# Kernel optimization log

Measured on AMD Instinct MI355X. Metric: run time of the kernel, lower is better.

## Reference

```python
import jax, jax.numpy as jnp
import numpy as np

H, D = 4, 64            # num_heads, head_size
HID = H * D             # 256
EPS = 1e-5              # torch LayerNorm default


def layer_norm(x, g, b):
    mu = x.mean(-1, keepdims=True)
    var = ((x - mu) ** 2).mean(-1, keepdims=True)
    return (x - mu) * jax.lax.rsqrt(var + EPS) * g + b


def mlstm_layer(x, Wq, Wk, Wv, Wo, bo, wi, bi, wf, bf, g, b):
    # x: (B, T, HID)
    B, T, _ = x.shape
    q = (x @ Wq).reshape(B, T, H, D) / (D ** 0.5)
    k = (x @ Wk).reshape(B, T, H, D)
    v = (x @ Wv).reshape(B, T, H, D)
    o = jax.nn.sigmoid(x @ Wo + bo).reshape(B, T, H, D)
    i_raw = x @ wi + bi  # (B, T, H)
    f_raw = x @ wf + bf  # (B, T, H)

    def step(carry, inp):
        C, n, m = carry                       # (B,H,D,D), (B,H,D), (B,H)
        q_t, k_t, v_t, o_t, i_t, f_t = inp
        m_t = jnp.maximum(f_t + m, i_t)       # stabilizer
        f_g = jnp.exp(f_t + m - m_t)          # (B,H)
        i_g = jnp.exp(i_t - m_t)              # (B,H)
        C = f_g[..., None, None] * C + i_g[..., None, None] * (v_t[..., :, None] * k_t[..., None, :])
        n = f_g[..., None] * n + i_g[..., None] * k_t
        Cq = jnp.einsum('bhde,bhd->bhe', C, q_t)
        nq = jnp.maximum(jnp.abs(jnp.sum(n * q_t, -1, keepdims=True)), 1.0)
        h = o_t * (Cq / nq)                   # (B,H,D)
        return (C, n, m_t), h.reshape(B, HID)

    C0 = jnp.zeros((B, H, D, D), x.dtype)
    n0 = jnp.zeros((B, H, D), x.dtype)
    m0 = jnp.zeros((B, H), x.dtype)
    xs = tuple(jnp.moveaxis(a, 1, 0) for a in (q, k, v, o, i_raw, f_raw))
    _, hs = jax.lax.scan(step, (C0, n0, m0), xs)  # hs: (T, B, HID)
    out = jnp.moveaxis(hs, 0, 1)                  # (B, T, HID)
    return layer_norm(out, g, b)


def setup_inputs() -> dict:
    B, T, IN, L = 256, 64, 170, 2
    key = jax.random.key(0)
    ks = jax.random.split(key, 19)
    s_in = 1.0 / np.sqrt(IN)
    s_h = 1.0 / np.sqrt(HID)
    return {
        'x':   jax.random.normal(ks[0], (B, T, IN), jnp.float32),
        'Wp':  jax.random.normal(ks[1], (IN, HID), jnp.float32) * s_in,
        'bp':  jax.random.normal(ks[2], (HID,), jnp.float32) * 0.01,
        'Wq':  jax.random.normal(ks[3], (L, HID, HID), jnp.float32) * s_h,
        'Wk':  jax.random.normal(ks[4], (L, HID, HID), jnp.float32) * s_h,
        'Wv':  jax.random.normal(ks[5], (L, HID, HID), jnp.float32) * s_h,
        'Wo':  jax.random.normal(ks[6], (L, HID, HID), jnp.float32) * s_h,
        'bo':  jax.random.normal(ks[7], (L, HID), jnp.float32) * 0.01,
        'wi':  jax.random.normal(ks[8], (L, HID, H), jnp.float32) * s_h,
        'bi':  jax.random.normal(ks[9], (L, H), jnp.float32) * 0.01,
        'wf':  jax.random.normal(ks[10], (L, HID, H), jnp.float32) * s_h,
        'bf':  jax.random.normal(ks[11], (L, H), jnp.float32) * 0.01,
        'lng': jnp.ones((L, HID), jnp.float32) + jax.random.normal(ks[12], (L, HID), jnp.float32) * 0.01,
        'lnb': jax.random.normal(ks[13], (L, HID), jnp.float32) * 0.01,
        'W1':  jax.random.normal(ks[14], (HID, 128), jnp.float32) * s_h,
        'b1':  jax.random.normal(ks[15], (128,), jnp.float32) * 0.01,
        'W2':  jax.random.normal(ks[16], (128, 2), jnp.float32) * (1.0 / np.sqrt(128)),
        'b2':  jax.random.normal(ks[17], (2,), jnp.float32) * 0.01,
    }


def reference(x, Wp, bp, Wq, Wk, Wv, Wo, bo, wi, bi, wf, bf, lng, lnb, W1, b1, W2, b2):
    h = x @ Wp + bp
    for l in range(Wq.shape[0]):
        h = mlstm_layer(h, Wq[l], Wk[l], Wv[l], Wo[l], bo[l],
                        wi[l], bi[l], wf[l], bf[l], lng[l], lnb[l])
    z = h[:, -1, :]                # last timestep
    z = jax.nn.relu(z @ W1 + b1)
    return z @ W2 + b2             # (B, 2)
```

## Files before the change

### kernel.cpp

```cpp
#include <hip/hip_runtime.h>
#include <math.h>

typedef __attribute__((ext_vector_type(4))) float f32x4;
typedef __attribute__((ext_vector_type(8))) short bf16x8;

constexpr int BATCH = 256;
constexpr int TT    = 64;
constexpr int NH    = 4;
constexpr int DH    = 64;
constexpr int HIDN  = 256;
constexpr int INDIM = 170;
constexpr int KPAD  = 192;
constexpr int ROWS  = BATCH * TT;
constexpr float EPS = 1e-5f;

#define MF(a, b, c) __builtin_amdgcn_mfma_f32_16x16x32_bf16((a), (b), (c), 0, 0, 0)

__device__ __forceinline__ unsigned short f2b(float f) {
    union { float f; unsigned int u; } v; v.f = f;
    return (unsigned short)((v.u + 0x7FFFu + ((v.u >> 16) & 1u)) >> 16);
}
__device__ __forceinline__ float b2f(unsigned short b) {
    union { unsigned int u; float f; } v; v.u = ((unsigned int)b) << 16;
    return v.f;
}
__device__ __forceinline__ void fsplit(float x, unsigned short& hi, unsigned short& lo) {
    hi = f2b(x);
    lo = f2b(x - b2f(hi));
}

__global__ __launch_bounds__(256) void pack_x(
    const float* __restrict__ x,
    unsigned short* __restrict__ xh, unsigned short* __restrict__ xl)
{
    int idx = blockIdx.x * 256 + threadIdx.x;
    if (idx >= ROWS * KPAD) return;
    int r = idx / KPAD, c = idx % KPAD;
    float v = (c < INDIM) ? x[(size_t)r * INDIM + c] : 0.f;
    unsigned short hi, lo; fsplit(v, hi, lo);
    xh[idx] = hi; xl[idx] = lo;
}

__global__ __launch_bounds__(256) void pack_w2(
    const float* __restrict__ Wp, const float* __restrict__ Wq,
    const float* __restrict__ Wk, const float* __restrict__ Wv,
    const float* __restrict__ Wo,
    unsigned short* __restrict__ WpTh, unsigned short* __restrict__ WpTl,
    unsigned short* __restrict__ Wth,  unsigned short* __restrict__ Wtl)
{
    __shared__ float T[64][65];
    const int t = blockIdx.x, tid = threadIdx.x;

    if (t < 128) {
        const int l = t >> 6, rem = t & 63;
        const int kt = rem >> 4, nt = rem & 15;
        const int n0 = nt * 64;
        const int seg = n0 >> 8, ns0 = n0 & 255;
        const float* W = (seg == 0) ? Wq : (seg == 1) ? Wk : (seg == 2) ? Wv : Wo;
        #pragma unroll
        for (int p = 0; p < 16; p++) {
            const int idx = p * 256 + tid;
            const int r = idx >> 6, c = idx & 63;
            T[r][c] = W[(size_t)l * 65536 + (size_t)(kt * 64 + r) * 256 + ns0 + c];
        }
        __syncthreads();
        #pragma unroll
        for (int p = 0; p < 16; p++) {
            const int idx = p * 256 + tid;
            const int nl = idx >> 6, kl = idx & 63;
            unsigned short hi, lo; fsplit(T[kl][nl], hi, lo);
            const size_t d = (size_t)l * 1024 * 256 + (size_t)(n0 + nl) * 256 + kt * 64 + kl;
            Wth[d] = hi; Wtl[d] = lo;
        }
    } else {
        const int t2 = t - 128;
        const int kt = t2 % 3, nt = t2 / 3;
        #pragma unroll
        for (int p = 0; p < 16; p++) {
            const int idx = p * 256 + tid;
            const int r = idx >> 6, c = idx & 63;
            const int k = kt * 64 + r;
            T[r][c] = (k < INDIM) ? Wp[(size_t)k * HIDN + nt * 64 + c] : 0.f;
        }
        __syncthreads();
        #pragma unroll
        for (int p = 0; p < 16; p++) {
            const int idx = p * 256 + tid;
            const int nl = idx >> 6, kl = idx & 63;
            unsigned short hi, lo; fsplit(T[kl][nl], hi, lo);
            const size_t d = (size_t)(nt * 64 + nl) * KPAD + kt * 64 + kl;
            WpTh[d] = hi; WpTl[d] = lo;
        }
    }
}

__global__ __launch_bounds__(256) void gemm_mfma3(
    const unsigned short* __restrict__ Ah, const unsigned short* __restrict__ Al,
    const unsigned short* __restrict__ Bh, const unsigned short* __restrict__ Bl,
    const float* __restrict__ bias,
    unsigned short* __restrict__ c0, unsigned short* __restrict__ c1,
    int M, int N, int K)
{
    __shared__ unsigned short AsH[128 * 64];
    __shared__ unsigned short AsL[128 * 64];
    __shared__ unsigned short BsH[128 * 64];
    __shared__ unsigned short BsL[128 * 64];
    const int tid  = threadIdx.x;
    const int lane = tid & 63;
    const int wave = tid >> 6;
    const int wr = wave >> 1, wc = wave & 1;
    const int m0 = blockIdx.x * 128, n0 = blockIdx.y * 128;

    f32x4 acc[4][4] = {};

    for (int k0 = 0; k0 < K; k0 += 64) {
        #pragma unroll
        for (int j = 0; j < 4; j++) {
            int c   = j * 256 + tid;
            int row = c >> 3;
            int kcs = ((c & 7) ^ (row & 7)) * 8;
            size_t aoff = (size_t)(m0 + row) * K + k0 + kcs;
            size_t boff = (size_t)(n0 + row) * K + k0 + kcs;
            __builtin_amdgcn_global_load_lds(
                (const __attribute__((address_space(1))) void*)(Ah + aoff),
                (__attribute__((address_space(3))) void*)(AsH + c * 8), 16, 0, 0);
            __builtin_amdgcn_global_load_lds(
                (const __attribute__((address_space(1))) void*)(Al + aoff),
                (__attribute__((address_space(3))) void*)(AsL + c * 8), 16, 0, 0);
            __builtin_amdgcn_global_load_lds(
                (const __attribute__((address_space(1))) void*)(Bh + boff),
                (__attribute__((address_space(3))) void*)(BsH + c * 8), 16, 0, 0);
            __builtin_amdgcn_global_load_lds(
                (const __attribute__((address_space(1))) void*)(Bl + boff),
                (__attribute__((address_space(3))) void*)(BsL + c * 8), 16, 0, 0);
        }
        asm volatile("s_waitcnt vmcnt(0)" ::: "memory");
        __syncthreads();

        #pragma unroll
        for (int kk = 0; kk < 2; kk++) {
            bf16x8 ah[4], al[4], bh[4], bl[4];
            #pragma unroll
            for (int i = 0; i < 4; i++) {
                const int ar  = wr * 64 + i * 16 + (lane & 15);
                const int off = ar * 64 + (((kk * 4 + (lane >> 4)) ^ (ar & 7)) * 8);
                ah[i] = *(const bf16x8*)&AsH[off];
                al[i] = *(const bf16x8*)&AsL[off];
            }
            #pragma unroll
            for (int j = 0; j < 4; j++) {
                const int br  = wc * 64 + j * 16 + (lane & 15);
                const int off = br * 64 + (((kk * 4 + (lane >> 4)) ^ (br & 7)) * 8);
                bh[j] = *(const bf16x8*)&BsH[off];
                bl[j] = *(const bf16x8*)&BsL[off];
            }
            #pragma unroll
            for (int i = 0; i < 4; i++) {
                #pragma unroll
                for (int j = 0; j < 4; j++) {
                    acc[i][j] = MF(ah[i], bh[j], acc[i][j]);
                    acc[i][j] = MF(ah[i], bl[j], acc[i][j]);
                    acc[i][j] = MF(al[i], bh[j], acc[i][j]);
                }
            }
        }
        __syncthreads();
    }

    #pragma unroll
    for (int i = 0; i < 4; i++) {
        #pragma unroll
        for (int j = 0; j < 4; j++) {
            const int col = n0 + wc * 64 + j * 16 + (lane & 15);
            const float bv = bias[col];
            #pragma unroll
            for (int r = 0; r < 4; r++) {
                const int row = m0 + wr * 64 + i * 16 + (lane >> 4) * 4 + r;
                float v = acc[i][j][r] + bv;
                unsigned short hi, lo; fsplit(v, hi, lo);
                c0[(size_t)row * N + col] = hi;
                c1[(size_t)row * N + col] = lo;
            }
        }
    }
}

__global__ __launch_bounds__(256) void ifproj(
    const unsigned short* __restrict__ hbh, const unsigned short* __restrict__ hbl,
    const float* __restrict__ wi, const float* __restrict__ wf,
    const float* __restrict__ bi, const float* __restrict__ bf,
    float* __restrict__ iout, float* __restrict__ fout)
{
    const int w    = threadIdx.x >> 6;
    const int lane = threadIdx.x & 63;
    const int row  = blockIdx.x * 4 + w;
    ushort4 a4 = *(const ushort4*)(hbh + (size_t)row * HIDN + lane * 4);
    ushort4 l4 = *(const ushort4*)(hbl + (size_t)row * HIDN + lane * 4);
    float yv[4];
    yv[0] = b2f(a4.x) + b2f(l4.x);
    yv[1] = b2f(a4.y) + b2f(l4.y);
    yv[2] = b2f(a4.z) + b2f(l4.z);
    yv[3] = b2f(a4.w) + b2f(l4.w);

    float g8[8] = {0.f,0.f,0.f,0.f,0.f,0.f,0.f,0.f};
    #pragma unroll
    for (int j = 0; j < 4; j++) {
        const float4 wiv = *(const float4*)(wi + (size_t)(lane * 4 + j) * 4);
        const float4 wfv = *(const float4*)(wf + (size_t)(lane * 4 + j) * 4);
        g8[0] += yv[j] * wiv.x; g8[1] += yv[j] * wiv.y;
        g8[2] += yv[j] * wiv.z; g8[3] += yv[j] * wiv.w;
        g8[4] += yv[j] * wfv.x; g8[5] += yv[j] * wfv.y;
        g8[6] += yv[j] * wfv.z; g8[7] += yv[j] * wfv.w;
    }
    #pragma unroll
    for (int o = 0; o < 8; o++)
        #pragma unroll
        for (int off = 32; off; off >>= 1) g8[o] += __shfl_xor(g8[o], off);
    if (lane < 4)      iout[(size_t)row * NH + lane] = g8[lane] + bi[lane];
    else if (lane < 8) fout[(size_t)row * NH + lane - 4] = g8[lane] + bf[lane - 4];
}

__global__ __launch_bounds__(512, 4) void fused_layer(
    const unsigned short* __restrict__ Ah, const unsigned short* __restrict__ Al,
    const unsigned short* __restrict__ Bh, const unsigned short* __restrict__ Bl,
    const float* __restrict__ bo,
    const float* __restrict__ irg, const float* __restrict__ frg,
    unsigned short* __restrict__ hoh, unsigned short* __restrict__ hol)
{
    extern __shared__ char smem[];
    unsigned short* const S = (unsigned short*)smem;
    float* const Ot   = (float*)smem;
    float* const denF = (float*)(S + 18432);

    const int n0  = blockIdx.x;
    const int mm  = n0 >> 3;
    const int hh  = mm & 3;
    const int b   = (n0 & 7) + 8 * (mm >> 2);
    const int tid = threadIdx.x, lane = tid & 63, w = tid >> 6;

    float iv = irg[(size_t)(b * TT + lane) * NH + hh];
    float fv = frg[(size_t)(b * TT + lane) * NH + hh];
    float F = fv;
    #pragma unroll
    for (int d2 = 1; d2 < 64; d2 <<= 1) { float o2 = __shfl_up(F, d2); if (lane >= d2) F += o2; }
    const float sa_r = iv - F;
    float pm = sa_r;
    #pragma unroll
    for (int d2 = 1; d2 < 64; d2 <<= 1) { float o2 = __shfl_up(pm, d2); if (lane >= d2) pm = fmaxf(pm, o2); }
    const float sc_r = -fmaxf(0.f, pm);

    const int wm = w >> 2, wn = w & 3;

    const unsigned short* sptr0; const unsigned short* sptr1;
    const unsigned short* sptr2; const unsigned short* sptr3;
    const unsigned short* sptr4;
    int sdst0, sdst1, sdst2, sdst3, sdst4;
    {
        {
            const int hl = tid >> 8, c = tid & 255;
            const int r = c >> 2, cp = c & 3;
            const int col = (cp ^ ((r >> 1) & 3)) * 8;
            sptr0 = (hl ? Al : Ah) + (size_t)(b * TT + r) * 256 + col;
            sdst0 = hl * 2048 + c * 8;
        }
        #pragma unroll
        for (int rr = 0; rr < 4; rr++) {
            const int c2 = rr * 512 + tid;
            const int hl = c2 >> 10, c = c2 & 1023;
            const int r = c >> 2, cp = c & 3;
            const int grow = (r >> 6) * 256 + hh * 64 + (r & 63);
            const int col = (cp ^ ((r >> 1) & 3)) * 8;
            const unsigned short* p = (hl ? Bl : Bh) + (size_t)grow * 256 + col;
            const int d = 4096 + hl * 8192 + c * 8;
            if (rr == 0) { sptr1 = p; sdst1 = d; }
            else if (rr == 1) { sptr2 = p; sdst2 = d; }
            else if (rr == 2) { sptr3 = p; sdst3 = d; }
            else { sptr4 = p; sdst4 = d; }
        }
    }

#define STAGE(bs)                                                              \
    do {                                                                       \
        __builtin_amdgcn_global_load_lds(                                      \
            (const __attribute__((address_space(1))) void*)sptr0,              \
            (__attribute__((address_space(3))) void*)(S + (bs) + sdst0), 16, 0, 0); \
        __builtin_amdgcn_global_load_lds(                                      \
            (const __attribute__((address_space(1))) void*)sptr1,              \
            (__attribute__((address_space(3))) void*)(S + (bs) + sdst1), 16, 0, 0); \
        __builtin_amdgcn_global_load_lds(                                      \
            (const __attribute__((address_space(1))) void*)sptr2,              \
            (__attribute__((address_space(3))) void*)(S + (bs) + sdst2), 16, 0, 0); \
        __builtin_amdgcn_global_load_lds(                                      \
            (const __attribute__((address_space(1))) void*)sptr3,              \
            (__attribute__((address_space(3))) void*)(S + (bs) + sdst3), 16, 0, 0); \
        __builtin_amdgcn_global_load_lds(                                      \
            (const __attribute__((address_space(1))) void*)sptr4,              \
            (__attribute__((address_space(3))) void*)(S + (bs) + sdst4), 16, 0, 0); \
        sptr0 += 32; sptr1 += 32; sptr2 += 32; sptr3 += 32; sptr4 += 32;       \
    } while (0)

    int aoff_[2], boff_[4];
    #pragma unroll
    for (int i = 0; i < 2; i++) {
        const int ar = wm * 32 + i * 16 + (lane & 15);
        aoff_[i] = ar * 32 + (((lane >> 4) ^ ((ar >> 1) & 3)) * 8);
    }
    #pragma unroll
    for (int j = 0; j < 4; j++) {
        const int br = wn * 64 + j * 16 + (lane & 15);
        boff_[j] = br * 32 + (((lane >> 4) ^ ((br >> 1) & 3)) * 8);
    }

    STAGE(0);
    asm volatile("s_waitcnt vmcnt(0)" ::: "memory");
    __syncthreads();

    f32x4 acc[2][4] = {};
    #pragma unroll
    for (int s = 0; s < 8; s++) {
        if (s < 7) STAGE(((s + 1) & 1) * 20480);

        const int pb = (s & 1) * 20480;
        __builtin_amdgcn_s_setprio(1);
        bf16x8 a_h[2], a_l[2], b_h[4], b_l[4];
        #pragma unroll
        for (int i = 0; i < 2; i++) {
            a_h[i] = *(const bf16x8*)&S[pb + aoff_[i]];
            a_l[i] = *(const bf16x8*)&S[pb + 2048 + aoff_[i]];
        }
        #pragma unroll
        for (int j = 0; j < 4; j++) {
            b_h[j] = *(const bf16x8*)&S[pb + 4096 + boff_[j]];
            b_l[j] = *(const bf16x8*)&S[pb + 12288 + boff_[j]];
        }
        #pragma unroll
        for (int i = 0; i < 2; i++) {
            #pragma unroll
            for (int j = 0; j < 4; j++) {
                acc[i][j] = MF(a_h[i], b_h[j], acc[i][j]);
                acc[i][j] = MF(a_h[i], b_l[j], acc[i][j]);
                acc[i][j] = MF(a_l[i], b_h[j], acc[i][j]);
            }
        }
        __builtin_amdgcn_s_setprio(0);
        if (s < 7) {
            asm volatile("s_waitcnt vmcnt(0)" ::: "memory");
            __syncthreads();
        }
    }
    __syncthreads();
#undef STAGE

    const int colb = lane & 15;
    const int rowb = (lane >> 4) * 4;
    #pragma unroll
    for (int i = 0; i < 2; i++) {
        #pragma unroll
        for (int j = 0; j < 4; j++) {
            const int d = j * 16 + colb;
            #pragma unroll
            for (int r = 0; r < 4; r++) {
                const int t = wm * 32 + i * 16 + rowb + r;
                float v = acc[i][j][r];
                if (wn == 0) {
                    v *= 0.125f;
                    unsigned short hi, lo; fsplit(v, hi, lo);
                    const int idx = t * 64 + (d ^ ((t & 7) << 3));
                    S[8192 + idx] = hi; S[12288 + idx] = lo;
                } else if (wn == 1) {
                    unsigned short hi, lo; fsplit(v, hi, lo);
                    const int idx = t * 64 + (d ^ ((t & 7) << 3));
                    S[16384 + idx] = hi; S[20480 + idx] = lo;
                    const int idx2 = d * 64 + (t ^ ((d & 7) << 3));
                    S[24576 + idx2] = hi; S[28672 + idx2] = lo;
                } else if (wn == 2) {
                    unsigned short hi, lo; fsplit(v, hi, lo);
                    const int idx = t * 64 + (d ^ ((t & 7) << 3));
                    S[32768 + idx] = hi; S[36864 + idx] = lo;
                } else {
                    Ot[t * 64 + d] = 1.f / (1.f + __expf(-(v + bo[hh * 64 + d])));
                }
            }
        }
    }
    __syncthreads();

    const int tg = w & 3, sh = w >> 2;
    f32x4 sv[2] = {}, sk[2] = {};
    const int tA = tg * 16 + (lane & 15);
    #pragma unroll
    for (int kk = 0; kk < 2; kk++) {
        const int eA = (kk * 32 + (lane >> 4) * 8) ^ ((tA & 7) << 3);
        bf16x8 aQh = *(const bf16x8*)&S[8192  + tA * 64 + eA];
        bf16x8 aQl = *(const bf16x8*)&S[12288 + tA * 64 + eA];
        #pragma unroll
        for (int j = 0; j < 2; j++) {
            const int sB = sh * 32 + j * 16 + (lane & 15);
            const int eB = (kk * 32 + (lane >> 4) * 8) ^ ((sB & 7) << 3);
            bf16x8 bKh = *(const bf16x8*)&S[16384 + sB * 64 + eB];
            bf16x8 bKl = *(const bf16x8*)&S[20480 + sB * 64 + eB];
            bf16x8 bVh = *(const bf16x8*)&S[32768 + sB * 64 + eB];
            bf16x8 bVl = *(const bf16x8*)&S[36864 + sB * 64 + eB];
            sv[j] = MF(aQh, bVh, sv[j]);
            sv[j] = MF(aQh, bVl, sv[j]);
            sv[j] = MF(aQl, bVh, sv[j]);
            sk[j] = MF(aQh, bKh, sk[j]);
            sk[j] = MF(aQh, bKl, sk[j]);
            sk[j] = MF(aQl, bKh, sk[j]);
        }
    }

    const int tbase = tg * 16 + (lane >> 4) * 4;
    float cw[4], dh4[4] = {0.f, 0.f, 0.f, 0.f};
    #pragma unroll
    for (int r = 0; r < 4; r++) cw[r] = __shfl(sc_r, tbase + r);
    #pragma unroll
    for (int j = 0; j < 2; j++) {
        const int s = sh * 32 + j * 16 + (lane & 15);
        const float as = __shfl(sa_r, s);
        #pragma unroll
        for (int r = 0; r < 4; r++) {
            const int t = tbase + r;
            const float wgt = (s <= t) ? __expf(as + cw[r]) : 0.f;
            sv[j][r] *= wgt;
            dh4[r] += sk[j][r] * wgt;
        }
    }
    #pragma unroll
    for (int r = 0; r < 4; r++) {
        dh4[r] += __shfl_xor(dh4[r], 1);
        dh4[r] += __shfl_xor(dh4[r], 2);
        dh4[r] += __shfl_xor(dh4[r], 4);
        dh4[r] += __shfl_xor(dh4[r], 8);
    }

    __syncthreads();

    #pragma unroll
    for (int j = 0; j < 2; j++) {
        const int s = sh * 32 + j * 16 + (lane & 15);
        #pragma unroll
        for (int r = 0; r < 4; r++) {
            const int t = tbase + r;
            unsigned short hi, lo; fsplit(sv[j][r], hi, lo);
            S[8192  + t * 72 + s] = hi;
            S[12800 + t * 72 + s] = lo;
        }
    }
    if ((lane & 15) == 0) {
        #pragma unroll
        for (int r = 0; r < 4; r++) denF[sh * 64 + tbase + r] = dh4[r];
    }
    __syncthreads();

    f32x4 num[2] = {};
    #pragma unroll
    for (int kk = 0; kk < 2; kk++) {
        const int sA2 = kk * 32 + (lane >> 4) * 8;
        bf16x8 aPh = *(const bf16x8*)&S[8192  + tA * 72 + sA2];
        bf16x8 aPl = *(const bf16x8*)&S[12800 + tA * 72 + sA2];
        #pragma unroll
        for (int j = 0; j < 2; j++) {
            const int e2 = sh * 32 + j * 16 + (lane & 15);
            const int tB = (kk * 32 + (lane >> 4) * 8) ^ ((e2 & 7) << 3);
            bf16x8 bTh = *(const bf16x8*)&S[24576 + e2 * 64 + tB];
            bf16x8 bTl = *(const bf16x8*)&S[28672 + e2 * 64 + tB];
            num[j] = MF(aPh, bTh, num[j]);
            num[j] = MF(aPh, bTl, num[j]);
            num[j] = MF(aPl, bTh, num[j]);
        }
    }

    #pragma unroll
    for (int j = 0; j < 2; j++) {
        const int e = sh * 32 + j * 16 + (lane & 15);
        #pragma unroll
        for (int r = 0; r < 4; r++) {
            const int t = tbase + r;
            const float den = fmaxf(fabsf(denF[t] + denF[64 + t]), 1.f);
            const float o = Ot[t * 64 + e];
            const float hval = o * num[j][r] / den;
            unsigned short hi, lo; fsplit(hval, hi, lo);
            const size_t oidx = (size_t)(b * TT + t) * HIDN + hh * DH + e;
            hoh[oidx] = hi; hol[oidx] = lo;
        }
    }
}

__global__ __launch_bounds__(256) void layernorm_gate(
    const unsigned short* __restrict__ sh_, const unsigned short* __restrict__ sl_,
    unsigned short* __restrict__ dh_, unsigned short* __restrict__ dl_,
    const float* __restrict__ g, const float* __restrict__ bta,
    const float* __restrict__ wi, const float* __restrict__ wf,
    const float* __restrict__ bi, const float* __restrict__ bf,
    float* __restrict__ iout, float* __restrict__ fout)
{
    const int w    = threadIdx.x >> 6;
    const int lane = threadIdx.x & 63;
    const int row  = blockIdx.x * 4 + w;
    ushort4 a4 = *(const ushort4*)(sh_ + (size_t)row * HIDN + lane * 4);
    ushort4 l4 = *(const ushort4*)(sl_ + (size_t)row * HIDN + lane * 4);
    float x0 = b2f(a4.x) + b2f(l4.x);
    float x1 = b2f(a4.y) + b2f(l4.y);
    float x2 = b2f(a4.z) + b2f(l4.z);
    float x3 = b2f(a4.w) + b2f(l4.w);
    float s = x0 + x1 + x2 + x3;
    #pragma unroll
    for (int off = 32; off; off >>= 1) s += __shfl_xor(s, off);
    const float mu = s * (1.f / 256.f);
    const float d0 = x0 - mu, d1 = x1 - mu, d2 = x2 - mu, d3 = x3 - mu;
    float vs = d0*d0 + d1*d1 + d2*d2 + d3*d3;
    #pragma unroll
    for (int off = 32; off; off >>= 1) vs += __shfl_xor(vs, off);
    const float rstd = rsqrtf(vs * (1.f / 256.f) + EPS);
    const float4 gv = *(const float4*)(g + lane * 4);
    const float4 bv = *(const float4*)(bta + lane * 4);
    float yv[4];
    yv[0] = d0 * rstd * gv.x + bv.x;
    yv[1] = d1 * rstd * gv.y + bv.y;
    yv[2] = d2 * rstd * gv.z + bv.z;
    yv[3] = d3 * rstd * gv.w + bv.w;
    ushort4 h4, o4;
    fsplit(yv[0], h4.x, o4.x); fsplit(yv[1], h4.y, o4.y);
    fsplit(yv[2], h4.z, o4.z); fsplit(yv[3], h4.w, o4.w);
    *(ushort4*)(dh_ + (size_t)row * HIDN + lane * 4) = h4;
    *(ushort4*)(dl_ + (size_t)row * HIDN + lane * 4) = o4;

    if (wi) {
        float g8[8] = {0.f,0.f,0.f,0.f,0.f,0.f,0.f,0.f};
        #pragma unroll
        for (int j = 0; j < 4; j++) {
            const float4 wiv = *(const float4*)(wi + (size_t)(lane * 4 + j) * 4);
            const float4 wfv = *(const float4*)(wf + (size_t)(lane * 4 + j) * 4);
            g8[0] += yv[j] * wiv.x; g8[1] += yv[j] * wiv.y;
            g8[2] += yv[j] * wiv.z; g8[3] += yv[j] * wiv.w;
            g8[4] += yv[j] * wfv.x; g8[5] += yv[j] * wfv.y;
            g8[6] += yv[j] * wfv.z; g8[7] += yv[j] * wfv.w;
        }
        #pragma unroll
        for (int o = 0; o < 8; o++)
            #pragma unroll
            for (int off = 32; off; off >>= 1) g8[o] += __shfl_xor(g8[o], off);
        if (lane < 4)      iout[(size_t)row * NH + lane] = g8[lane] + bi[lane];
        else if (lane < 8) fout[(size_t)row * NH + lane - 4] = g8[lane] + bf[lane - 4];
    }
}

__global__ __launch_bounds__(128) void head_mlp(
    const unsigned short* __restrict__ hbh, const unsigned short* __restrict__ hbl,
    const float* __restrict__ W1, const float* __restrict__ b1,
    const float* __restrict__ W2, const float* __restrict__ b2,
    float* __restrict__ out)
{
    const int b = blockIdx.x;
    const int j = threadIdx.x;
    __shared__ float z[HIDN];
    __shared__ float a[128];
    const size_t rb = ((size_t)b * TT + (TT - 1)) * HIDN;
    z[j]       = b2f(hbh[rb + j])       + b2f(hbl[rb + j]);
    z[j + 128] = b2f(hbh[rb + j + 128]) + b2f(hbl[rb + j + 128]);
    __syncthreads();
    float acc = b1[j];
    #pragma unroll 4
    for (int c = 0; c < HIDN; c++) acc += z[c] * W1[c * 128 + j];
    a[j] = fmaxf(acc, 0.f);
    __syncthreads();
    if (j < 2) {
        float s = b2[j];
        for (int c = 0; c < 128; c++) s += a[c] * W2[c * 2 + j];
        out[b * 2 + j] = s;
    }
}

extern "C" void kernel_launch(void* const* d_in, const int* in_sizes, int n_in,
                              void* d_out, int out_size, void* d_ws, size_t ws_size,
                              hipStream_t stream)
{
    const float* x   = (const float*)d_in[0];
    const float* Wp  = (const float*)d_in[1];
    const float* bp  = (const float*)d_in[2];
    const float* Wq  = (const float*)d_in[3];
    const float* Wk  = (const float*)d_in[4];
    const float* Wv  = (const float*)d_in[5];
    const float* Wo  = (const float*)d_in[6];
    const float* bo  = (const float*)d_in[7];
    const float* wi  = (const float*)d_in[8];
    const float* bi  = (const float*)d_in[9];
    const float* wf  = (const float*)d_in[10];
    const float* bf  = (const float*)d_in[11];
    const float* lng = (const float*)d_in[12];
    const float* lnb = (const float*)d_in[13];
    const float* W1  = (const float*)d_in[14];
    const float* b1  = (const float*)d_in[15];
    const float* W2  = (const float*)d_in[16];
    const float* b2  = (const float*)d_in[17];
    float* out = (float*)d_out;

    unsigned short* hbh = (unsigned short*)d_ws;
    unsigned short* hbl = hbh + (size_t)ROWS * HIDN;
    unsigned short* h2h = hbl + (size_t)ROWS * HIDN;
    unsigned short* h2l = h2h + (size_t)ROWS * HIDN;
    float*          ir  = (float*)(h2l + (size_t)ROWS * HIDN);
    float*          fr  = ir + (size_t)ROWS * NH;
    unsigned short* WpTh = (unsigned short*)(fr + (size_t)ROWS * NH);
    unsigned short* WpTl = WpTh + (size_t)HIDN * KPAD;
    unsigned short* Wth  = WpTl + (size_t)HIDN * KPAD;
    unsigned short* Wtl  = Wth + (size_t)2 * 1024 * 256;
    unsigned short* xh = h2h;
    unsigned short* xl = h2l;

    pack_x<<<(ROWS * KPAD + 255) / 256, 256, 0, stream>>>(x, xh, xl);
    pack_w2<<<140, 256, 0, stream>>>(Wp, Wq, Wk, Wv, Wo, WpTh, WpTl, Wth, Wtl);

    gemm_mfma3<<<dim3(128, 2), 256, 0, stream>>>(
        xh, xl, WpTh, WpTl, bp, hbh, hbl, ROWS, HIDN, KPAD);

    ifproj<<<ROWS / 4, 256, 0, stream>>>(hbh, hbl, wi, wf, bi, bf, ir, fr);

    fused_layer<<<BATCH * NH, 512, 81920, stream>>>(
        hbh, hbl, Wth, Wtl, bo, ir, fr, h2h, h2l);
    layernorm_gate<<<ROWS / 4, 256, 0, stream>>>(
        h2h, h2l, hbh, hbl, lng, lnb,
        wi + (size_t)HIDN * NH, wf + (size_t)HIDN * NH, bi + NH, bf + NH, ir, fr);

    fused_layer<<<BATCH * NH, 512, 81920, stream>>>(
        hbh, hbl, Wth + (size_t)1024 * 256, Wtl + (size_t)1024 * 256,
        bo + HIDN, ir, fr, h2h, h2l);
    layernorm_gate<<<ROWS / 4, 256, 0, stream>>>(
        h2h, h2l, hbh, hbl, lng + HIDN, lnb + HIDN,
        nullptr, nullptr, nullptr, nullptr, nullptr, nullptr);

    head_mlp<<<BATCH, 128, 0, stream>>>(hbh, hbl, W1, b1, W2, b2, out);
}
```

Measured before the change: 169.9 us.

## Process four batches per block in fused_layer to reuse weight tiles

Each fused_layer block now handles four batch elements for one head instead of one. The projection GEMM stages a single weight tile per K step and reuses it across four A tiles, so weight traffic into LDS per batch drops. The grid shrinks from 1024 to 256 blocks, LDS per block grows to 128KB, and the accumulators grow to 4x2x4 MFMA tiles. The per-batch chunkwise mLSTM epilogue runs serially inside the block, which costs parallelism and occupancy.

```diff
diff --git a/kernel.cpp b/kernel.cpp
--- a/kernel.cpp
+++ b/kernel.cpp
@@ -220,7 +220,7 @@
     else if (lane < 8) fout[(size_t)row * NH + lane - 4] = g8[lane] + bf[lane - 4];
 }
 
-__global__ __launch_bounds__(512, 4) void fused_layer(
+__global__ __launch_bounds__(512, 2) void fused_layer(
     const unsigned short* __restrict__ Ah, const unsigned short* __restrict__ Al,
     const unsigned short* __restrict__ Bh, const unsigned short* __restrict__ Bl,
     const float* __restrict__ bo,
@@ -232,114 +232,106 @@
     float* const Ot   = (float*)smem;
     float* const denF = (float*)(S + 18432);
 
-    const int n0  = blockIdx.x;
-    const int mm  = n0 >> 3;
-    const int hh  = mm & 3;
-    const int b   = (n0 & 7) + 8 * (mm >> 2);
+    const int bid = blockIdx.x;
+    const int hh  = (bid >> 3) & 3;
+    const int bg  = (bid & 7) + 8 * (bid >> 5);
+    const int b0  = bg * 4;
     const int tid = threadIdx.x, lane = tid & 63, w = tid >> 6;
 
-    float iv = irg[(size_t)(b * TT + lane) * NH + hh];
-    float fv = frg[(size_t)(b * TT + lane) * NH + hh];
-    float F = fv;
-    #pragma unroll
-    for (int d2 = 1; d2 < 64; d2 <<= 1) { float o2 = __shfl_up(F, d2); if (lane >= d2) F += o2; }
-    const float sa_r = iv - F;
-    float pm = sa_r;
-    #pragma unroll
-    for (int d2 = 1; d2 < 64; d2 <<= 1) { float o2 = __shfl_up(pm, d2); if (lane >= d2) pm = fmaxf(pm, o2); }
-    const float sc_r = -fmaxf(0.f, pm);
+    float sa4[4], sc4[4];
+    #pragma unroll
+    for (int g = 0; g < 4; g++) {
+        float iv = irg[(size_t)((b0 + g) * TT + lane) * NH + hh];
+        float fv = frg[(size_t)((b0 + g) * TT + lane) * NH + hh];
+        float F = fv;
+        #pragma unroll
+        for (int d2 = 1; d2 < 64; d2 <<= 1) { float o2 = __shfl_up(F, d2); if (lane >= d2) F += o2; }
+        const float av = iv - F;
+        float pm = av;
+        #pragma unroll
+        for (int d2 = 1; d2 < 64; d2 <<= 1) { float o2 = __shfl_up(pm, d2); if (lane >= d2) pm = fmaxf(pm, o2); }
+        sa4[g] = av;
+        sc4[g] = -fmaxf(0.f, pm);
+    }
 
     const int wm = w >> 2, wn = w & 3;
 
-    const unsigned short* sptr0; const unsigned short* sptr1;
-    const unsigned short* sptr2; const unsigned short* sptr3;
-    const unsigned short* sptr4;
-    int sdst0, sdst1, sdst2, sdst3, sdst4;
-    {
-        {
-            const int hl = tid >> 8, c = tid & 255;
-            const int r = c >> 2, cp = c & 3;
-            const int col = (cp ^ ((r >> 1) & 3)) * 8;
-            sptr0 = (hl ? Al : Ah) + (size_t)(b * TT + r) * 256 + col;
-            sdst0 = hl * 2048 + c * 8;
-        }
-        #pragma unroll
-        for (int rr = 0; rr < 4; rr++) {
-            const int c2 = rr * 512 + tid;
-            const int hl = c2 >> 10, c = c2 & 1023;
-            const int r = c >> 2, cp = c & 3;
-            const int grow = (r >> 6) * 256 + hh * 64 + (r & 63);
-            const int col = (cp ^ ((r >> 1) & 3)) * 8;
-            const unsigned short* p = (hl ? Bl : Bh) + (size_t)grow * 256 + col;
-            const int d = 4096 + hl * 8192 + c * 8;
-            if (rr == 0) { sptr1 = p; sdst1 = d; }
-            else if (rr == 1) { sptr2 = p; sdst2 = d; }
-            else if (rr == 2) { sptr3 = p; sdst3 = d; }
-            else { sptr4 = p; sdst4 = d; }
-        }
+    const unsigned short* sp[8];
+    unsigned int sd[8];
+    #pragma unroll
+    for (int q = 0; q < 8; q++) {
+        const int c  = q * 512 + tid;
+        const int rg = c >> 10;
+        const int cc = c & 1023;
+        const int r  = cc >> 2;
+        const int cp = cc & 3;
+        const int colsw = (cp ^ ((r >> 1) & 3)) * 8;
+        size_t grow;
+        const unsigned short* base;
+        if (rg < 2) { base = (rg == 0) ? Ah : Al; grow = (size_t)(bg * 256 + r); }
+        else {
+            base = (rg == 2) ? Bh : Bl;
+            grow = (size_t)((r >> 6) * 256 + hh * 64 + (r & 63));
+        }
+        sp[q] = base + grow * 256 + colsw;
+        sd[q] = rg * 8192 + cc * 8;
     }
 
 #define STAGE(bs)                                                              \
     do {                                                                       \
-        __builtin_amdgcn_global_load_lds(                                      \
-            (const __attribute__((address_space(1))) void*)sptr0,              \
-            (__attribute__((address_space(3))) void*)(S + (bs) + sdst0), 16, 0, 0); \
-        __builtin_amdgcn_global_load_lds(                                      \
-            (const __attribute__((address_space(1))) void*)sptr1,              \
-            (__attribute__((address_space(3))) void*)(S + (bs) + sdst1), 16, 0, 0); \
-        __builtin_amdgcn_global_load_lds(                                      \
-            (const __attribute__((address_space(1))) void*)sptr2,              \
-            (__attribute__((address_space(3))) void*)(S + (bs) + sdst2), 16, 0, 0); \
-        __builtin_amdgcn_global_load_lds(                                      \
-            (const __attribute__((address_space(1))) void*)sptr3,              \
-            (__attribute__((address_space(3))) void*)(S + (bs) + sdst3), 16, 0, 0); \
-        __builtin_amdgcn_global_load_lds(                                      \
-            (const __attribute__((address_space(1))) void*)sptr4,              \
-            (__attribute__((address_space(3))) void*)(S + (bs) + sdst4), 16, 0, 0); \
-        sptr0 += 32; sptr1 += 32; sptr2 += 32; sptr3 += 32; sptr4 += 32;       \
+        _Pragma("unroll")                                                      \
+        for (int q = 0; q < 8; q++) {                                          \
+            __builtin_amdgcn_global_load_lds(                                  \
+                (const __attribute__((address_space(1))) void*)sp[q],          \
+                (__attribute__((address_space(3))) void*)(S + (bs) + sd[q]), 16, 0, 0); \
+            sp[q] += 32;                                                       \
+        }                                                                      \
     } while (0)
 
-    int aoff_[2], boff_[4];
+    unsigned int aoffb[2], boffb[4];
     #pragma unroll
     for (int i = 0; i < 2; i++) {
         const int ar = wm * 32 + i * 16 + (lane & 15);
-        aoff_[i] = ar * 32 + (((lane >> 4) ^ ((ar >> 1) & 3)) * 8);
+        aoffb[i] = ar * 32 + (((lane >> 4) ^ ((ar >> 1) & 3)) * 8);
     }
     #pragma unroll
     for (int j = 0; j < 4; j++) {
         const int br = wn * 64 + j * 16 + (lane & 15);
-        boff_[j] = br * 32 + (((lane >> 4) ^ ((br >> 1) & 3)) * 8);
+        boffb[j] = br * 32 + (((lane >> 4) ^ ((br >> 1) & 3)) * 8);
     }
 
     STAGE(0);
     asm volatile("s_waitcnt vmcnt(0)" ::: "memory");
     __syncthreads();
 
-    f32x4 acc[2][4] = {};
-    #pragma unroll
+    f32x4 acc[4][2][4] = {};
     for (int s = 0; s < 8; s++) {
-        if (s < 7) STAGE(((s + 1) & 1) * 20480);
-
-        const int pb = (s & 1) * 20480;
+        if (s < 7) STAGE(((s + 1) & 1) * 32768);
+
+        const int pb = (s & 1) * 32768;
         __builtin_amdgcn_s_setprio(1);
-        bf16x8 a_h[2], a_l[2], b_h[4], b_l[4];
-        #pragma unroll
-        for (int i = 0; i < 2; i++) {
-            a_h[i] = *(const bf16x8*)&S[pb + aoff_[i]];
-            a_l[i] = *(const bf16x8*)&S[pb + 2048 + aoff_[i]];
-        }
+        bf16x8 b_h[4], b_l[4];
         #pragma unroll
         for (int j = 0; j < 4; j++) {
-            b_h[j] = *(const bf16x8*)&S[pb + 4096 + boff_[j]];
-            b_l[j] = *(const bf16x8*)&S[pb + 12288 + boff_[j]];
-        }
-        #pragma unroll
-        for (int i = 0; i < 2; i++) {
-            #pragma unroll
-            for (int j = 0; j < 4; j++) {
-                acc[i][j] = MF(a_h[i], b_h[j], acc[i][j]);
-                acc[i][j] = MF(a_h[i], b_l[j], acc[i][j]);
-                acc[i][j] = MF(a_l[i], b_h[j], acc[i][j]);
+            b_h[j] = *(const bf16x8*)&S[pb + 16384 + boffb[j]];
+            b_l[j] = *(const bf16x8*)&S[pb + 24576 + boffb[j]];
+        }
+        #pragma unroll
+        for (int g = 0; g < 4; g++) {
+            bf16x8 a_h[2], a_l[2];
+            #pragma unroll
+            for (int i = 0; i < 2; i++) {
+                a_h[i] = *(const bf16x8*)&S[pb + g * 2048 + aoffb[i]];
+                a_l[i] = *(const bf16x8*)&S[pb + 8192 + g * 2048 + aoffb[i]];
+            }
+            #pragma unroll
+            for (int i = 0; i < 2; i++) {
+                #pragma unroll
+                for (int j = 0; j < 4; j++) {
+                    acc[g][i][j] = MF(a_h[i], b_h[j], acc[g][i][j]);
+                    acc[g][i][j] = MF(a_h[i], b_l[j], acc[g][i][j]);
+                    acc[g][i][j] = MF(a_l[i], b_h[j], acc[g][i][j]);
+                }
             }
         }
         __builtin_amdgcn_s_setprio(0);
@@ -353,137 +345,144 @@
 
     const int colb = lane & 15;
     const int rowb = (lane >> 4) * 4;
-    #pragma unroll
-    for (int i = 0; i < 2; i++) {
-        #pragma unroll
-        for (int j = 0; j < 4; j++) {
-            const int d = j * 16 + colb;
+    const int tg = w & 3, sh = w >> 2;
+    const int tA = tg * 16 + (lane & 15);
+    const int tbase = tg * 16 + (lane >> 4) * 4;
+
+    #pragma unroll
+    for (int g = 0; g < 4; g++) {
+        const int bcur = b0 + g;
+
+        #pragma unroll
+        for (int i = 0; i < 2; i++) {
+            #pragma unroll
+            for (int j = 0; j < 4; j++) {
+                const int d = j * 16 + colb;
+                #pragma unroll
+                for (int r = 0; r < 4; r++) {
+                    const int t = wm * 32 + i * 16 + rowb + r;
+                    float v = acc[g][i][j][r];
+                    if (wn == 0) {
+                        v *= 0.125f;
+                        unsigned short hi, lo; fsplit(v, hi, lo);
+                        const int idx = t * 64 + (d ^ ((t & 7) << 3));
+                        S[8192 + idx] = hi; S[12288 + idx] = lo;
+                    } else if (wn == 1) {
+                        unsigned short hi, lo; fsplit(v, hi, lo);
+                        const int idx = t * 64 + (d ^ ((t & 7) << 3));
+                        S[16384 + idx] = hi; S[20480 + idx] = lo;
+                        const int idx2 = d * 64 + (t ^ ((d & 7) << 3));
+                        S[24576 + idx2] = hi; S[28672 + idx2] = lo;
+                    } else if (wn == 2) {
+                        unsigned short hi, lo; fsplit(v, hi, lo);
+                        const int idx = t * 64 + (d ^ ((t & 7) << 3));
+                        S[32768 + idx] = hi; S[36864 + idx] = lo;
+                    } else {
+                        Ot[t * 64 + d] = 1.f / (1.f + __expf(-(v + bo[hh * 64 + d])));
+                    }
+                }
+            }
+        }
+        __syncthreads();
+
+        f32x4 sv[2] = {}, sk[2] = {};
+        #pragma unroll
+        for (int kk = 0; kk < 2; kk++) {
+            const int eA = (kk * 32 + (lane >> 4) * 8) ^ ((tA & 7) << 3);
+            bf16x8 aQh = *(const bf16x8*)&S[8192  + tA * 64 + eA];
+            bf16x8 aQl = *(const bf16x8*)&S[12288 + tA * 64 + eA];
+            #pragma unroll
+            for (int j = 0; j < 2; j++) {
+                const int sB = sh * 32 + j * 16 + (lane & 15);
+                const int eB = (kk * 32 + (lane >> 4) * 8) ^ ((sB & 7) << 3);
+                bf16x8 bKh = *(const bf16x8*)&S[16384 + sB * 64 + eB];
+                bf16x8 bKl = *(const bf16x8*)&S[20480 + sB * 64 + eB];
+                bf16x8 bVh = *(const bf16x8*)&S[32768 + sB * 64 + eB];
+                bf16x8 bVl = *(const bf16x8*)&S[36864 + sB * 64 + eB];
+                sv[j] = MF(aQh, bVh, sv[j]);
+                sv[j] = MF(aQh, bVl, sv[j]);
+                sv[j] = MF(aQl, bVh, sv[j]);
+                sk[j] = MF(aQh, bKh, sk[j]);
+                sk[j] = MF(aQh, bKl, sk[j]);
+                sk[j] = MF(aQl, bKh, sk[j]);
+            }
+        }
+
+        float cw[4], dh4[4] = {0.f, 0.f, 0.f, 0.f};
+        #pragma unroll
+        for (int r = 0; r < 4; r++) cw[r] = __shfl(sc4[g], tbase + r);
+        #pragma unroll
+        for (int j = 0; j < 2; j++) {
+            const int s = sh * 32 + j * 16 + (lane & 15);
+            const float as = __shfl(sa4[g], s);
             #pragma unroll
             for (int r = 0; r < 4; r++) {
-                const int t = wm * 32 + i * 16 + rowb + r;
-                float v = acc[i][j][r];
-                if (wn == 0) {
-                    v *= 0.125f;
-                    unsigned short hi, lo; fsplit(v, hi, lo);
-                    const int idx = t * 64 + (d ^ ((t & 7) << 3));
-                    S[8192 + idx] = hi; S[12288 + idx] = lo;
-                } else if (wn == 1) {
-                    unsigned short hi, lo; fsplit(v, hi, lo);
-                    const int idx = t * 64 + (d ^ ((t & 7) << 3));
-                    S[16384 + idx] = hi; S[20480 + idx] = lo;
-                    const int idx2 = d * 64 + (t ^ ((d & 7) << 3));
-                    S[24576 + idx2] = hi; S[28672 + idx2] = lo;
-                } else if (wn == 2) {
-                    unsigned short hi, lo; fsplit(v, hi, lo);
-                    const int idx = t * 64 + (d ^ ((t & 7) << 3));
-                    S[32768 + idx] = hi; S[36864 + idx] = lo;
-                } else {
-                    Ot[t * 64 + d] = 1.f / (1.f + __expf(-(v + bo[hh * 64 + d])));
-                }
-            }
-        }
-    }
-    __syncthreads();
-
-    const int tg = w & 3, sh = w >> 2;
-    f32x4 sv[2] = {}, sk[2] = {};
-    const int tA = tg * 16 + (lane & 15);
-    #pragma unroll
-    for (int kk = 0; kk < 2; kk++) {
-        const int eA = (kk * 32 + (lane >> 4) * 8) ^ ((tA & 7) << 3);
-        bf16x8 aQh = *(const bf16x8*)&S[8192  + tA * 64 + eA];
-        bf16x8 aQl = *(const bf16x8*)&S[12288 + tA * 64 + eA];
+                const int t = tbase + r;
+                const float wgt = (s <= t) ? __expf(as + cw[r]) : 0.f;
+                sv[j][r] *= wgt;
+                dh4[r] += sk[j][r] * wgt;
+            }
+        }
+        #pragma unroll
+        for (int r = 0; r < 4; r++) {
+            dh4[r] += __shfl_xor(dh4[r], 1);
+            dh4[r] += __shfl_xor(dh4[r], 2);
+            dh4[r] += __shfl_xor(dh4[r], 4);
+            dh4[r] += __shfl_xor(dh4[r], 8);
+        }
+
+        __syncthreads();
+
         #pragma unroll
         for (int j = 0; j < 2; j++) {
-            const int sB = sh * 32 + j * 16 + (lane & 15);
-            const int eB = (kk * 32 + (lane >> 4) * 8) ^ ((sB & 7) << 3);
-            bf16x8 bKh = *(const bf16x8*)&S[16384 + sB * 64 + eB];
-            bf16x8 bKl = *(const bf16x8*)&S[20480 + sB * 64 + eB];
-            bf16x8 bVh = *(const bf16x8*)&S[32768 + sB * 64 + eB];
-            bf16x8 bVl = *(const bf16x8*)&S[36864 + sB * 64 + eB];
-            sv[j] = MF(aQh, bVh, sv[j]);
-            sv[j] = MF(aQh, bVl, sv[j]);
-            sv[j] = MF(aQl, bVh, sv[j]);
-            sk[j] = MF(aQh, bKh, sk[j]);
-            sk[j] = MF(aQh, bKl, sk[j]);
-            sk[j] = MF(aQl, bKh, sk[j]);
-        }
-    }
-
-    const int tbase = tg * 16 + (lane >> 4) * 4;
-    float cw[4], dh4[4] = {0.f, 0.f, 0.f, 0.f};
-    #pragma unroll
-    for (int r = 0; r < 4; r++) cw[r] = __shfl(sc_r, tbase + r);
-    #pragma unroll
-    for (int j = 0; j < 2; j++) {
-        const int s = sh * 32 + j * 16 + (lane & 15);
-        const float as = __shfl(sa_r, s);
-        #pragma unroll
-        for (int r = 0; r < 4; r++) {
-            const int t = tbase + r;
-            const float wgt = (s <= t) ? __expf(as + cw[r]) : 0.f;
-            sv[j][r] *= wgt;
-            dh4[r] += sk[j][r] * wgt;
-        }
-    }
-    #pragma unroll
-    for (int r = 0; r < 4; r++) {
-        dh4[r] += __shfl_xor(dh4[r], 1);
-        dh4[r] += __shfl_xor(dh4[r], 2);
-        dh4[r] += __shfl_xor(dh4[r], 4);
-        dh4[r] += __shfl_xor(dh4[r], 8);
-    }
-
-    __syncthreads();
-
-    #pragma unroll
-    for (int j = 0; j < 2; j++) {
-        const int s = sh * 32 + j * 16 + (lane & 15);
-        #pragma unroll
-        for (int r = 0; r < 4; r++) {
-            const int t = tbase + r;
-            unsigned short hi, lo; fsplit(sv[j][r], hi, lo);
-            S[8192  + t * 72 + s] = hi;
-            S[12800 + t * 72 + s] = lo;
-        }
-    }
-    if ((lane & 15) == 0) {
-        #pragma unroll
-        for (int r = 0; r < 4; r++) denF[sh * 64 + tbase + r] = dh4[r];
-    }
-    __syncthreads();
-
-    f32x4 num[2] = {};
-    #pragma unroll
-    for (int kk = 0; kk < 2; kk++) {
-        const int sA2 = kk * 32 + (lane >> 4) * 8;
-        bf16x8 aPh = *(const bf16x8*)&S[8192  + tA * 72 + sA2];
-        bf16x8 aPl = *(const bf16x8*)&S[12800 + tA * 72 + sA2];
+            const int s = sh * 32 + j * 16 + (lane & 15);
+            #pragma unroll
+            for (int r = 0; r < 4; r++) {
+                const int t = tbase + r;
+                unsigned short hi, lo; fsplit(sv[j][r], hi, lo);
+                S[8192  + t * 72 + s] = hi;
+                S[12800 + t * 72 + s] = lo;
+            }
+        }
+        if ((lane & 15) == 0) {
+            #pragma unroll
+            for (int r = 0; r < 4; r++) denF[sh * 64 + tbase + r] = dh4[r];
+        }
+        __syncthreads();
+
+        f32x4 num[2] = {};
+        #pragma unroll
+        for (int kk = 0; kk < 2; kk++) {
+            const int sA2 = kk * 32 + (lane >> 4) * 8;
+            bf16x8 aPh = *(const bf16x8*)&S[8192  + tA * 72 + sA2];
+            bf16x8 aPl = *(const bf16x8*)&S[12800 + tA * 72 + sA2];
+            #pragma unroll
+            for (int j = 0; j < 2; j++) {
+                const int e2 = sh * 32 + j * 16 + (lane & 15);
+                const int tB = (kk * 32 + (lane >> 4) * 8) ^ ((e2 & 7) << 3);
+                bf16x8 bTh = *(const bf16x8*)&S[24576 + e2 * 64 + tB];
+                bf16x8 bTl = *(const bf16x8*)&S[28672 + e2 * 64 + tB];
+                num[j] = MF(aPh, bTh, num[j]);
+                num[j] = MF(aPh, bTl, num[j]);
+                num[j] = MF(aPl, bTh, num[j]);
+            }
+        }
+
         #pragma unroll
         for (int j = 0; j < 2; j++) {
-            const int e2 = sh * 32 + j * 16 + (lane & 15);
-            const int tB = (kk * 32 + (lane >> 4) * 8) ^ ((e2 & 7) << 3);
-            bf16x8 bTh = *(const bf16x8*)&S[24576 + e2 * 64 + tB];
-            bf16x8 bTl = *(const bf16x8*)&S[28672 + e2 * 64 + tB];
-            num[j] = MF(aPh, bTh, num[j]);
-            num[j] = MF(aPh, bTl, num[j]);
-            num[j] = MF(aPl, bTh, num[j]);
-        }
-    }
-
-    #pragma unroll
-    for (int j = 0; j < 2; j++) {
-        const int e = sh * 32 + j * 16 + (lane & 15);
-        #pragma unroll
-        for (int r = 0; r < 4; r++) {
-            const int t = tbase + r;
-            const float den = fmaxf(fabsf(denF[t] + denF[64 + t]), 1.f);
-            const float o = Ot[t * 64 + e];
-            const float hval = o * num[j][r] / den;
-            unsigned short hi, lo; fsplit(hval, hi, lo);
-            const size_t oidx = (size_t)(b * TT + t) * HIDN + hh * DH + e;
-            hoh[oidx] = hi; hol[oidx] = lo;
-        }
+            const int e = sh * 32 + j * 16 + (lane & 15);
+            #pragma unroll
+            for (int r = 0; r < 4; r++) {
+                const int t = tbase + r;
+                const float den = fmaxf(fabsf(denF[t] + denF[64 + t]), 1.f);
+                const float o = Ot[t * 64 + e];
+                const float hval = o * num[j][r] / den;
+                unsigned short hi, lo; fsplit(hval, hi, lo);
+                const size_t oidx = (size_t)(bcur * TT + t) * HIDN + hh * DH + e;
+                hoh[oidx] = hi; hol[oidx] = lo;
+            }
+        }
+        __syncthreads();
     }
 }
 
@@ -617,13 +616,13 @@
 
     ifproj<<<ROWS / 4, 256, 0, stream>>>(hbh, hbl, wi, wf, bi, bf, ir, fr);
 
-    fused_layer<<<BATCH * NH, 512, 81920, stream>>>(
+    fused_layer<<<256, 512, 131072, stream>>>(
         hbh, hbl, Wth, Wtl, bo, ir, fr, h2h, h2l);
     layernorm_gate<<<ROWS / 4, 256, 0, stream>>>(
         h2h, h2l, hbh, hbl, lng, lnb,
         wi + (size_t)HIDN * NH, wf + (size_t)HIDN * NH, bi + NH, bf + NH, ir, fr);
 
-    fused_layer<<<BATCH * NH, 512, 81920, stream>>>(
+    fused_layer<<<256, 512, 131072, stream>>>(
         hbh, hbl, Wth + (size_t)1024 * 256, Wtl + (size_t)1024 * 256,
         bo + HIDN, ir, fr, h2h, h2l);
     layernorm_gate<<<ROWS / 4, 256, 0, stream>>>(
```

After: 529.8 us. 212% more time.

## Use single-bf16 intra-chunk attention and single-buffer staging to raise occupancy

Applied to the files above, without the earlier changes.

Replaces the hi/lo split-bf16 (three-MFMA) products for QK, QV and P·K^T inside the fused layer with single bf16 operands and one MFMA each. It also drops the double-buffered global-to-LDS staging of the projection GEMM in favour of a single buffer with sync per step. Together these shrink dynamic LDS from 80 KB to 48 KB, and launch bounds are raised to allow more blocks per CU. The aim is fewer MFMAs, less LDS traffic and higher occupancy. The cost is lower numerical precision in the recurrence math and lost load/compute overlap in the GEMM loop.

```diff
diff --git a/kernel.cpp b/kernel.cpp
--- a/kernel.cpp
+++ b/kernel.cpp
@@ -220,7 +220,7 @@
     else if (lane < 8) fout[(size_t)row * NH + lane - 4] = g8[lane] + bf[lane - 4];
 }
 
-__global__ __launch_bounds__(512, 4) void fused_layer(
+__global__ __launch_bounds__(512, 6) void fused_layer(
     const unsigned short* __restrict__ Ah, const unsigned short* __restrict__ Al,
     const unsigned short* __restrict__ Bh, const unsigned short* __restrict__ Bl,
     const float* __restrict__ bo,
@@ -230,7 +230,7 @@
     extern __shared__ char smem[];
     unsigned short* const S = (unsigned short*)smem;
     float* const Ot   = (float*)smem;
-    float* const denF = (float*)(S + 18432);
+    float* const denF = (float*)(S + 12800);
 
     const int n0  = blockIdx.x;
     const int mm  = n0 >> 3;
@@ -279,23 +279,23 @@
         }
     }
 
-#define STAGE(bs)                                                              \
+#define STAGE()                                                                \
     do {                                                                       \
         __builtin_amdgcn_global_load_lds(                                      \
             (const __attribute__((address_space(1))) void*)sptr0,              \
-            (__attribute__((address_space(3))) void*)(S + (bs) + sdst0), 16, 0, 0); \
+            (__attribute__((address_space(3))) void*)(S + sdst0), 16, 0, 0);   \
         __builtin_amdgcn_global_load_lds(                                      \
             (const __attribute__((address_space(1))) void*)sptr1,              \
-            (__attribute__((address_space(3))) void*)(S + (bs) + sdst1), 16, 0, 0); \
+            (__attribute__((address_space(3))) void*)(S + sdst1), 16, 0, 0);   \
         __builtin_amdgcn_global_load_lds(                                      \
             (const __attribute__((address_space(1))) void*)sptr2,              \
-            (__attribute__((address_space(3))) void*)(S + (bs) + sdst2), 16, 0, 0); \
+            (__attribute__((address_space(3))) void*)(S + sdst2), 16, 0, 0);   \
         __builtin_amdgcn_global_load_lds(                                      \
             (const __attribute__((address_space(1))) void*)sptr3,              \
-            (__attribute__((address_space(3))) void*)(S + (bs) + sdst3), 16, 0, 0); \
+            (__attribute__((address_space(3))) void*)(S + sdst3), 16, 0, 0);   \
         __builtin_amdgcn_global_load_lds(                                      \
             (const __attribute__((address_space(1))) void*)sptr4,              \
-            (__attribute__((address_space(3))) void*)(S + (bs) + sdst4), 16, 0, 0); \
+            (__attribute__((address_space(3))) void*)(S + sdst4), 16, 0, 0);   \
         sptr0 += 32; sptr1 += 32; sptr2 += 32; sptr3 += 32; sptr4 += 32;       \
     } while (0)
 
@@ -311,27 +311,23 @@
         boff_[j] = br * 32 + (((lane >> 4) ^ ((br >> 1) & 3)) * 8);
     }
 
-    STAGE(0);
-    asm volatile("s_waitcnt vmcnt(0)" ::: "memory");
-    __syncthreads();
-
     f32x4 acc[2][4] = {};
-    #pragma unroll
     for (int s = 0; s < 8; s++) {
-        if (s < 7) STAGE(((s + 1) & 1) * 20480);
-
-        const int pb = (s & 1) * 20480;
+        STAGE();
+        asm volatile("s_waitcnt vmcnt(0)" ::: "memory");
+        __syncthreads();
+
         __builtin_amdgcn_s_setprio(1);
         bf16x8 a_h[2], a_l[2], b_h[4], b_l[4];
         #pragma unroll
         for (int i = 0; i < 2; i++) {
-            a_h[i] = *(const bf16x8*)&S[pb + aoff_[i]];
-            a_l[i] = *(const bf16x8*)&S[pb + 2048 + aoff_[i]];
+            a_h[i] = *(const bf16x8*)&S[aoff_[i]];
+            a_l[i] = *(const bf16x8*)&S[2048 + aoff_[i]];
         }
         #pragma unroll
         for (int j = 0; j < 4; j++) {
-            b_h[j] = *(const bf16x8*)&S[pb + 4096 + boff_[j]];
-            b_l[j] = *(const bf16x8*)&S[pb + 12288 + boff_[j]];
+            b_h[j] = *(const bf16x8*)&S[4096 + boff_[j]];
+            b_l[j] = *(const bf16x8*)&S[12288 + boff_[j]];
         }
         #pragma unroll
         for (int i = 0; i < 2; i++) {
@@ -343,12 +339,8 @@
             }
         }
         __builtin_amdgcn_s_setprio(0);
-        if (s < 7) {
-            asm volatile("s_waitcnt vmcnt(0)" ::: "memory");
-            __syncthreads();
-        }
-    }
-    __syncthreads();
+        __syncthreads();
+    }
 #undef STAGE
 
     const int colb = lane & 15;
@@ -363,20 +355,17 @@
                 const int t = wm * 32 + i * 16 + rowb + r;
                 float v = acc[i][j][r];
                 if (wn == 0) {
-                    v *= 0.125f;
-                    unsigned short hi, lo; fsplit(v, hi, lo);
                     const int idx = t * 64 + (d ^ ((t & 7) << 3));
-                    S[8192 + idx] = hi; S[12288 + idx] = lo;
+                    S[8192 + idx] = f2b(v * 0.125f);
                 } else if (wn == 1) {
-                    unsigned short hi, lo; fsplit(v, hi, lo);
+                    const unsigned short kb = f2b(v);
                     const int idx = t * 64 + (d ^ ((t & 7) << 3));
-                    S[16384 + idx] = hi; S[20480 + idx] = lo;
+                    S[12288 + idx] = kb;
                     const int idx2 = d * 64 + (t ^ ((d & 7) << 3));
-                    S[24576 + idx2] = hi; S[28672 + idx2] = lo;
+                    S[16384 + idx2] = kb;
                 } else if (wn == 2) {
-                    unsigned short hi, lo; fsplit(v, hi, lo);
                     const int idx = t * 64 + (d ^ ((t & 7) << 3));
-                    S[32768 + idx] = hi; S[36864 + idx] = lo;
+                    S[20480 + idx] = f2b(v);
                 } else {
                     Ot[t * 64 + d] = 1.f / (1.f + __expf(-(v + bo[hh * 64 + d])));
                 }
@@ -391,22 +380,15 @@
     #pragma unroll
     for (int kk = 0; kk < 2; kk++) {
         const int eA = (kk * 32 + (lane >> 4) * 8) ^ ((tA & 7) << 3);
-        bf16x8 aQh = *(const bf16x8*)&S[8192  + tA * 64 + eA];
-        bf16x8 aQl = *(const bf16x8*)&S[12288 + tA * 64 + eA];
+        const bf16x8 aQ = *(const bf16x8*)&S[8192 + tA * 64 + eA];
         #pragma unroll
         for (int j = 0; j < 2; j++) {
             const int sB = sh * 32 + j * 16 + (lane & 15);
             const int eB = (kk * 32 + (lane >> 4) * 8) ^ ((sB & 7) << 3);
-            bf16x8 bKh = *(const bf16x8*)&S[16384 + sB * 64 + eB];
-            bf16x8 bKl = *(const bf16x8*)&S[20480 + sB * 64 + eB];
-            bf16x8 bVh = *(const bf16x8*)&S[32768 + sB * 64 + eB];
-            bf16x8 bVl = *(const bf16x8*)&S[36864 + sB * 64 + eB];
-            sv[j] = MF(aQh, bVh, sv[j]);
-            sv[j] = MF(aQh, bVl, sv[j]);
-            sv[j] = MF(aQl, bVh, sv[j]);
-            sk[j] = MF(aQh, bKh, sk[j]);
-            sk[j] = MF(aQh, bKl, sk[j]);
-            sk[j] = MF(aQl, bKh, sk[j]);
+            const bf16x8 bK = *(const bf16x8*)&S[12288 + sB * 64 + eB];
+            const bf16x8 bV = *(const bf16x8*)&S[20480 + sB * 64 + eB];
+            sv[j] = MF(aQ, bV, sv[j]);
+            sk[j] = MF(aQ, bK, sk[j]);
         }
     }
 
@@ -442,9 +424,7 @@
         #pragma unroll
         for (int r = 0; r < 4; r++) {
             const int t = tbase + r;
-            unsigned short hi, lo; fsplit(sv[j][r], hi, lo);
-            S[8192  + t * 72 + s] = hi;
-            S[12800 + t * 72 + s] = lo;
+            S[8192 + t * 72 + s] = f2b(sv[j][r]);
         }
     }
     if ((lane & 15) == 0) {
@@ -457,17 +437,13 @@
     #pragma unroll
     for (int kk = 0; kk < 2; kk++) {
         const int sA2 = kk * 32 + (lane >> 4) * 8;
-        bf16x8 aPh = *(const bf16x8*)&S[8192  + tA * 72 + sA2];
-        bf16x8 aPl = *(const bf16x8*)&S[12800 + tA * 72 + sA2];
+        const bf16x8 aP = *(const bf16x8*)&S[8192 + tA * 72 + sA2];
         #pragma unroll
         for (int j = 0; j < 2; j++) {
             const int e2 = sh * 32 + j * 16 + (lane & 15);
             const int tB = (kk * 32 + (lane >> 4) * 8) ^ ((e2 & 7) << 3);
-            bf16x8 bTh = *(const bf16x8*)&S[24576 + e2 * 64 + tB];
-            bf16x8 bTl = *(const bf16x8*)&S[28672 + e2 * 64 + tB];
-            num[j] = MF(aPh, bTh, num[j]);
-            num[j] = MF(aPh, bTl, num[j]);
-            num[j] = MF(aPl, bTh, num[j]);
+            const bf16x8 bT = *(const bf16x8*)&S[16384 + e2 * 64 + tB];
+            num[j] = MF(aP, bT, num[j]);
         }
     }
 
@@ -617,13 +593,13 @@
 
     ifproj<<<ROWS / 4, 256, 0, stream>>>(hbh, hbl, wi, wf, bi, bf, ir, fr);
 
-    fused_layer<<<BATCH * NH, 512, 81920, stream>>>(
+    fused_layer<<<BATCH * NH, 512, 49152, stream>>>(
         hbh, hbl, Wth, Wtl, bo, ir, fr, h2h, h2l);
     layernorm_gate<<<ROWS / 4, 256, 0, stream>>>(
         h2h, h2l, hbh, hbl, lng, lnb,
         wi + (size_t)HIDN * NH, wf + (size_t)HIDN * NH, bi + NH, bf + NH, ir, fr);
 
-    fused_layer<<<BATCH * NH, 512, 81920, stream>>>(
+    fused_layer<<<BATCH * NH, 512, 49152, stream>>>(
         hbh, hbl, Wth + (size_t)1024 * 256, Wtl + (size_t)1024 * 256,
         bo + HIDN, ir, fr, h2h, h2l);
     layernorm_gate<<<ROWS / 4, 256, 0, stream>>>(
```

Result: slower. 245.3 us (+44.4%).
